# Performance work log

Hardware: AMD Instinct MI355X
Metric: run time of the kernel (lower is better)

Reference implementation:

```python
import jax, jax.numpy as jnp
import numpy as np
import math

B, H, N, D = 4, 8, 2048, 64


def setup_inputs() -> dict:
    key = jax.random.key(0)
    kq, kk, kv = jax.random.split(key, 3)
    q = jax.random.normal(kq, (B, H, N, D), dtype=jnp.float32)
    k = jax.random.normal(kk, (B, H, N, D), dtype=jnp.float32)
    v = jax.random.normal(kv, (B, H, N, D), dtype=jnp.float32)
    return {"q": q, "k": k, "v": v}


def reference(q, k, v):
    # global_attention_Sub: expanded squared L2 distance ||q_i - k_j||^2
    # = qq_i - 2 q_i.k_j + kk_j, then softmax(-dist/sqrt(D)) @ v.
    scale = math.sqrt(q.shape[-1])
    inner = -2.0 * jnp.einsum('bhnd,bhmd->bhnm', q, k)          # [B,H,N,N]
    qq = jnp.sum(q * q, axis=-1, keepdims=True)                  # [B,H,N,1]
    kk = jnp.sum(k * k, axis=-1, keepdims=True)                  # [B,H,N,1]
    diff_sq = qq + inner + jnp.swapaxes(kk, -1, -2)              # [B,H,N,N]
    attn = jax.nn.softmax(-diff_sq / scale, axis=-1)
    x = jnp.einsum('bhnm,bhmd->bhnd', attn, v)                   # [B,H,N,D]
    return jnp.transpose(x, (0, 2, 1, 3))                        # [B,N,H,D]
```

## Files before the change

kernel.cpp:

```cpp
#include <hip/hip_runtime.h>

typedef __bf16 bf16x4 __attribute__((ext_vector_type(4)));
typedef __bf16 bf16x8 __attribute__((ext_vector_type(8)));
typedef float floatx4 __attribute__((ext_vector_type(4)));

constexpr int Bc = 4, Hc = 8, Nc = 2048, Dc = 64;
constexpr int BQ = 128;
constexpr int WQ = 16;
constexpr int TK = 64;
constexpr int NT = Nc / TK;
constexpr int SPS = 72;
constexpr float LOG2E = 1.44269504088896340736f;

constexpr size_t KSW_OFF = 0;
constexpr size_t VSW_OFF = (size_t)32 * NT * 8192;
constexpr size_t KKN_OFF = VSW_OFF * 2;

typedef __attribute__((address_space(1))) const unsigned int gu32;
typedef __attribute__((address_space(3))) unsigned int lu32;
__device__ __forceinline__ void dma16(const void* g, void* l) {
    __builtin_amdgcn_global_load_lds((gu32*)g, (lu32*)l, 16, 0, 0);
}
__device__ __forceinline__ void dma4(const void* g, void* l) {
    __builtin_amdgcn_global_load_lds((gu32*)g, (lu32*)l, 4, 0, 0);
}

__global__ __launch_bounds__(256) void prep_kernel(
    const float* __restrict__ Kg, const float* __restrict__ Vg, char* __restrict__ ws)
{
    __shared__ float sT[64 * 68];
    const int tid = threadIdx.x;
    const int jt = blockIdx.x, bh = blockIdx.y;

    __bf16* Ksw = (__bf16*)(ws + KSW_OFF) + ((size_t)bh * NT + jt) * 4096;
    __bf16* Vsw = (__bf16*)(ws + VSW_OFF) + ((size_t)bh * NT + jt) * 4096;
    float*  kkn = (float*)(ws + KKN_OFF) + (size_t)bh * Nc + jt * 64;
    const size_t tb = ((size_t)bh * Nc + jt * 64) * Dc;

#pragma unroll
    for (int cc = 0; cc < 2; ++cc) {
        const int g   = tid + cc * 256;
        const int key = g >> 3, kcx = g & 7;
        const int kc  = kcx ^ (key & 7);
        const float* src = Kg + tb + key * 64 + kc * 8;
        float4 a = *(const float4*)src;
        float4 b = *(const float4*)(src + 4);
        float ss = a.x*a.x + a.y*a.y + a.z*a.z + a.w*a.w
                 + b.x*b.x + b.y*b.y + b.z*b.z + b.w*b.w;
        ss += __shfl_xor(ss, 1);
        ss += __shfl_xor(ss, 2);
        ss += __shfl_xor(ss, 4);
        if (kcx == 0) kkn[key] = -(ss * 0.125f * LOG2E);
        bf16x8 c8;
        c8[0]=(__bf16)a.x; c8[1]=(__bf16)a.y; c8[2]=(__bf16)a.z; c8[3]=(__bf16)a.w;
        c8[4]=(__bf16)b.x; c8[5]=(__bf16)b.y; c8[6]=(__bf16)b.z; c8[7]=(__bf16)b.w;
        *(bf16x8*)(Ksw + g * 8) = c8;
    }
    {
        const int js = tid >> 2, dc = (tid & 3) * 16;
        const float* vr = Vg + tb + js * 64 + dc;
        float* dst = &sT[js * 68 + dc];
        *(float4*)dst       = *(const float4*)vr;
        *(float4*)(dst + 4) = *(const float4*)(vr + 4);
        *(float4*)(dst + 8) = *(const float4*)(vr + 8);
        *(float4*)(dst + 12)= *(const float4*)(vr + 12);
    }
    __syncthreads();
#pragma unroll
    for (int cc = 0; cc < 2; ++cc) {
        const int g = tid + cc * 256;
        const int d = g >> 3, kcx = g & 7;
        const int kc = kcx ^ (d & 7);
        bf16x8 c8;
#pragma unroll
        for (int e = 0; e < 8; ++e) {
            const int ee = (e + kcx) & 7;
            c8[ee] = (__bf16)sT[(kc * 8 + ee) * 68 + d];
        }
        *(bf16x8*)(Vsw + g * 8) = c8;
    }
}

__global__ __launch_bounds__(512, 4) void attn_kernel(
    const float* __restrict__ Qg, const char* __restrict__ ws, float* __restrict__ Og)
{
    __shared__ __align__(16) __bf16 sK[2][4096];
    __shared__ __align__(16) __bf16 sVall[3 * 4096];
    __shared__ __align__(16) float  skk[2][64];
    __shared__ __align__(16) __bf16 sP[BQ * SPS];
    __shared__ __align__(16) float  sl[BQ];

    const int tid  = threadIdx.x;
    const int wave = tid >> 6;
    const int lane = tid & 63;
    const int qd   = lane >> 4;
    const int c    = lane & 15;

    const int qt = blockIdx.x;
    const int bh = blockIdx.y;

    const char* Kimg = ws + KSW_OFF + (size_t)bh * NT * 8192;
    const char* Vimg = ws + VSW_OFF + (size_t)bh * NT * 8192;
    const float* kkp = (const float*)(ws + KKN_OFF) + (size_t)bh * Nc;

    const float qscale = 0.25f * LOG2E;
    const int i0 = qt * BQ + wave * WQ;

    bf16x8 qf[2];
    {
        const float* qrow = Qg + ((size_t)bh * Nc + i0 + c) * Dc + qd * 8;
#pragma unroll
        for (int ks = 0; ks < 2; ++ks) {
            float4 a = *(const float4*)(qrow + ks * 32);
            float4 b = *(const float4*)(qrow + ks * 32 + 4);
            bf16x8 f;
            f[0] = (__bf16)(a.x * qscale); f[1] = (__bf16)(a.y * qscale);
            f[2] = (__bf16)(a.z * qscale); f[3] = (__bf16)(a.w * qscale);
            f[4] = (__bf16)(b.x * qscale); f[5] = (__bf16)(b.y * qscale);
            f[6] = (__bf16)(b.z * qscale); f[7] = (__bf16)(b.w * qscale);
            qf[ks] = f;
        }
    }

    const int koff0 = c * 64 + ((qd ^ (c & 7)) << 3);
    const int koff1 = c * 64 + (((4 + qd) ^ (c & 7)) << 3);

    floatx4 oacc[4];
#pragma unroll
    for (int dt = 0; dt < 4; ++dt)
#pragma unroll
        for (int e = 0; e < 4; ++e) oacc[dt][e] = 0.f;
    float lp = 0.f;

    __bf16* vprev = &sVall[2 * 4096];
    __bf16* vcur  = &sVall[0];
    __bf16* vnext = &sVall[1 * 4096];

    auto stage = [&](int jt2, int kb, __bf16* vdst) {
        const char* ki = Kimg + (size_t)jt2 * 8192;
        const char* vi = Vimg + (size_t)jt2 * 8192;
        const int off = tid * 16;
        dma16(ki + off, (char*)&sK[kb][0] + off);
        dma16(vi + off, (char*)vdst + off);
        if (wave == 7) dma4(kkp + jt2 * 64 + lane, &skk[kb][0]);
    };

    stage(0, 0, vcur);

    bf16x8 pfp[2];

    for (int jt = 0; jt < NT; ++jt) {
        const int b = jt & 1;
        __syncthreads();
        if (jt + 1 < NT) stage(jt + 1, b ^ 1, vnext);

        floatx4 st[4];
#pragma unroll
        for (int kt = 0; kt < 4; ++kt)
            st[kt] = *(const floatx4*)&skk[b][kt * 16 + qd * 4];
#pragma unroll
        for (int kt = 0; kt < 4; ++kt) {
            const __bf16* kbase = &sK[b][kt * 1024];
            bf16x8 kf0 = *(const bf16x8*)(kbase + koff0);
            bf16x8 kf1 = *(const bf16x8*)(kbase + koff1);
            st[kt] = __builtin_amdgcn_mfma_f32_16x16x32_bf16(kf0, qf[0], st[kt], 0, 0, 0);
            st[kt] = __builtin_amdgcn_mfma_f32_16x16x32_bf16(kf1, qf[1], st[kt], 0, 0, 0);
        }

        if (jt > 0) {
#pragma unroll
            for (int dt = 0; dt < 4; ++dt) {
                const __bf16* vbase = vprev + dt * 1024;
                bf16x8 vf0 = *(const bf16x8*)(vbase + koff0);
                bf16x8 vf1 = *(const bf16x8*)(vbase + koff1);
                oacc[dt] = __builtin_amdgcn_mfma_f32_16x16x32_bf16(pfp[0], vf0, oacc[dt], 0, 0, 0);
                oacc[dt] = __builtin_amdgcn_mfma_f32_16x16x32_bf16(pfp[1], vf1, oacc[dt], 0, 0, 0);
            }
        }

        {
            const int prow = wave * WQ + c;
#pragma unroll
            for (int kt = 0; kt < 4; ++kt) {
                float p0 = __builtin_amdgcn_exp2f(st[kt][0]);
                float p1 = __builtin_amdgcn_exp2f(st[kt][1]);
                float p2 = __builtin_amdgcn_exp2f(st[kt][2]);
                float p3 = __builtin_amdgcn_exp2f(st[kt][3]);
                lp += (p0 + p1) + (p2 + p3);
                bf16x4 pk;
                pk[0] = (__bf16)p0; pk[1] = (__bf16)p1;
                pk[2] = (__bf16)p2; pk[3] = (__bf16)p3;
                *(bf16x4*)&sP[prow * SPS + kt * 16 + qd * 4] = pk;
            }
        }
#pragma unroll
        for (int ks = 0; ks < 2; ++ks)
            pfp[ks] = *(const bf16x8*)&sP[(wave * WQ + c) * SPS + ks * 32 + qd * 8];

        __bf16* t = vprev; vprev = vcur; vcur = vnext; vnext = t;
    }

#pragma unroll
    for (int dt = 0; dt < 4; ++dt) {
        const __bf16* vbase = vprev + dt * 1024;
        bf16x8 vf0 = *(const bf16x8*)(vbase + koff0);
        bf16x8 vf1 = *(const bf16x8*)(vbase + koff1);
        oacc[dt] = __builtin_amdgcn_mfma_f32_16x16x32_bf16(pfp[0], vf0, oacc[dt], 0, 0, 0);
        oacc[dt] = __builtin_amdgcn_mfma_f32_16x16x32_bf16(pfp[1], vf1, oacc[dt], 0, 0, 0);
    }

    {
        float l = lp;
        l += __shfl_xor(l, 16);
        l += __shfl_xor(l, 32);
        if (qd == 0) sl[wave * WQ + c] = l;
    }
    const int b_ = bh >> 3, hh = bh & 7;
    {
        floatx4 lf = *(const floatx4*)&sl[wave * WQ + qd * 4];
#pragma unroll
        for (int r = 0; r < 4; ++r) {
            const float inv = 1.f / lf[r];
            const int i = i0 + qd * 4 + r;
            float* orow = Og + (((size_t)b_ * Nc + i) * Hc + hh) * Dc + c;
#pragma unroll
            for (int dt = 0; dt < 4; ++dt)
                orow[dt * 16] = oacc[dt][r] * inv;
        }
    }
}

extern "C" void kernel_launch(void* const* d_in, const int* in_sizes, int n_in,
                              void* d_out, int out_size, void* d_ws, size_t ws_size,
                              hipStream_t stream) {
    const float* q = (const float*)d_in[0];
    const float* k = (const float*)d_in[1];
    const float* v = (const float*)d_in[2];
    float* out = (float*)d_out;
    char* ws = (char*)d_ws;
    prep_kernel<<<dim3(NT, Bc * Hc), 256, 0, stream>>>(k, v, ws);
    attn_kernel<<<dim3(Nc / BQ, Bc * Hc), 512, 0, stream>>>(q, ws, out);
}
```

Before: 136.9 us.

## Switch attention to 32x32 MFMA with in-register P via permlane32 swap

Moves the attention kernel from 16x16x32 to 32x32x16 bf16 MFMA, with 4 waves of 32 query rows each instead of 8 waves of 16. The probability tile no longer goes through shared memory: it is packed to bf16 and rearranged between lane halves with v_permlane32_swap, then used directly as the A operand of the PV MFMA. The key-norm bias is written by prep in a permuted order matching the 32x32 accumulator layout and read straight from global memory rather than staged through LDS. This removes the sP LDS round trip and the one-tile-delayed PV pipeline, in exchange for more registers per wave and half as many waves per block.

```diff
diff --git a/kernel.cpp b/kernel.cpp
--- a/kernel.cpp
+++ b/kernel.cpp
@@ -1,15 +1,15 @@
 #include <hip/hip_runtime.h>
 
-typedef __bf16 bf16x4 __attribute__((ext_vector_type(4)));
 typedef __bf16 bf16x8 __attribute__((ext_vector_type(8)));
 typedef float floatx4 __attribute__((ext_vector_type(4)));
+typedef float floatx16 __attribute__((ext_vector_type(16)));
+typedef unsigned int uintx4 __attribute__((ext_vector_type(4)));
 
 constexpr int Bc = 4, Hc = 8, Nc = 2048, Dc = 64;
 constexpr int BQ = 128;
-constexpr int WQ = 16;
+constexpr int WQ = 32;
 constexpr int TK = 64;
 constexpr int NT = Nc / TK;
-constexpr int SPS = 72;
 constexpr float LOG2E = 1.44269504088896340736f;
 
 constexpr size_t KSW_OFF = 0;
@@ -21,8 +21,11 @@
 __device__ __forceinline__ void dma16(const void* g, void* l) {
     __builtin_amdgcn_global_load_lds((gu32*)g, (lu32*)l, 16, 0, 0);
 }
-__device__ __forceinline__ void dma4(const void* g, void* l) {
-    __builtin_amdgcn_global_load_lds((gu32*)g, (lu32*)l, 4, 0, 0);
+
+__device__ __forceinline__ unsigned pk2(float lo, float hi) {
+    unsigned short a = __builtin_bit_cast(unsigned short, (__bf16)lo);
+    unsigned short b = __builtin_bit_cast(unsigned short, (__bf16)hi);
+    return (unsigned)a | ((unsigned)b << 16);
 }
 
 __global__ __launch_bounds__(256) void prep_kernel(
@@ -50,7 +53,11 @@
         ss += __shfl_xor(ss, 1);
         ss += __shfl_xor(ss, 2);
         ss += __shfl_xor(ss, 4);
-        if (kcx == 0) kkn[key] = -(ss * 0.125f * LOG2E);
+        if (kcx == 0) {
+            const int k5 = key & 31, kt = key >> 5;
+            const int rlo = k5 & 3, hh = (k5 >> 2) & 1, rhi = k5 >> 3;
+            kkn[kt * 32 + hh * 16 + rhi * 4 + rlo] = -(ss * 0.125f * LOG2E);
+        }
         bf16x8 c8;
         c8[0]=(__bf16)a.x; c8[1]=(__bf16)a.y; c8[2]=(__bf16)a.z; c8[3]=(__bf16)a.w;
         c8[4]=(__bf16)b.x; c8[5]=(__bf16)b.y; c8[6]=(__bf16)b.z; c8[7]=(__bf16)b.w;
@@ -81,20 +88,18 @@
     }
 }
 
-__global__ __launch_bounds__(512, 4) void attn_kernel(
+__global__ __launch_bounds__(256, 4) void attn_kernel(
     const float* __restrict__ Qg, const char* __restrict__ ws, float* __restrict__ Og)
 {
     __shared__ __align__(16) __bf16 sK[2][4096];
-    __shared__ __align__(16) __bf16 sVall[3 * 4096];
-    __shared__ __align__(16) float  skk[2][64];
-    __shared__ __align__(16) __bf16 sP[BQ * SPS];
+    __shared__ __align__(16) __bf16 sV[2][4096];
     __shared__ __align__(16) float  sl[BQ];
 
     const int tid  = threadIdx.x;
     const int wave = tid >> 6;
     const int lane = tid & 63;
-    const int qd   = lane >> 4;
-    const int c    = lane & 15;
+    const int r31  = lane & 31;
+    const int hi   = lane >> 5;
 
     const int qt = blockIdx.x;
     const int bh = blockIdx.y;
@@ -106,13 +111,13 @@
     const float qscale = 0.25f * LOG2E;
     const int i0 = qt * BQ + wave * WQ;
 
-    bf16x8 qf[2];
+    bf16x8 qf[4];
     {
-        const float* qrow = Qg + ((size_t)bh * Nc + i0 + c) * Dc + qd * 8;
-#pragma unroll
-        for (int ks = 0; ks < 2; ++ks) {
-            float4 a = *(const float4*)(qrow + ks * 32);
-            float4 b = *(const float4*)(qrow + ks * 32 + 4);
+        const float* qrow = Qg + ((size_t)bh * Nc + i0 + r31) * Dc + hi * 8;
+#pragma unroll
+        for (int ks = 0; ks < 4; ++ks) {
+            float4 a = *(const float4*)(qrow + ks * 16);
+            float4 b = *(const float4*)(qrow + ks * 16 + 4);
             bf16x8 f;
             f[0] = (__bf16)(a.x * qscale); f[1] = (__bf16)(a.y * qscale);
             f[2] = (__bf16)(a.z * qscale); f[3] = (__bf16)(a.w * qscale);
@@ -122,110 +127,105 @@
         }
     }
 
-    const int koff0 = c * 64 + ((qd ^ (c & 7)) << 3);
-    const int koff1 = c * 64 + (((4 + qd) ^ (c & 7)) << 3);
-
-    floatx4 oacc[4];
-#pragma unroll
-    for (int dt = 0; dt < 4; ++dt)
-#pragma unroll
-        for (int e = 0; e < 4; ++e) oacc[dt][e] = 0.f;
-    float lp = 0.f;
-
-    __bf16* vprev = &sVall[2 * 4096];
-    __bf16* vcur  = &sVall[0];
-    __bf16* vnext = &sVall[1 * 4096];
-
-    auto stage = [&](int jt2, int kb, __bf16* vdst) {
+    int off4[4];
+#pragma unroll
+    for (int ks = 0; ks < 4; ++ks)
+        off4[ks] = r31 * 128 + (((ks * 2 + hi) ^ (r31 & 7)) << 4);
+
+    floatx16 oacc[2];
+#pragma unroll
+    for (int dt = 0; dt < 2; ++dt)
+#pragma unroll
+        for (int e = 0; e < 16; ++e) oacc[dt][e] = 0.f;
+    float lpr = 0.f;
+
+    auto stage = [&](int jt2, int nb) {
         const char* ki = Kimg + (size_t)jt2 * 8192;
         const char* vi = Vimg + (size_t)jt2 * 8192;
         const int off = tid * 16;
-        dma16(ki + off, (char*)&sK[kb][0] + off);
-        dma16(vi + off, (char*)vdst + off);
-        if (wave == 7) dma4(kkp + jt2 * 64 + lane, &skk[kb][0]);
+        dma16(ki + off,        (char*)&sK[nb][0] + off);
+        dma16(ki + off + 4096, (char*)&sK[nb][0] + off + 4096);
+        dma16(vi + off,        (char*)&sV[nb][0] + off);
+        dma16(vi + off + 4096, (char*)&sV[nb][0] + off + 4096);
     };
 
-    stage(0, 0, vcur);
-
-    bf16x8 pfp[2];
+    stage(0, 0);
 
     for (int jt = 0; jt < NT; ++jt) {
         const int b = jt & 1;
         __syncthreads();
-        if (jt + 1 < NT) stage(jt + 1, b ^ 1, vnext);
-
-        floatx4 st[4];
-#pragma unroll
-        for (int kt = 0; kt < 4; ++kt)
-            st[kt] = *(const floatx4*)&skk[b][kt * 16 + qd * 4];
-#pragma unroll
-        for (int kt = 0; kt < 4; ++kt) {
-            const __bf16* kbase = &sK[b][kt * 1024];
-            bf16x8 kf0 = *(const bf16x8*)(kbase + koff0);
-            bf16x8 kf1 = *(const bf16x8*)(kbase + koff1);
-            st[kt] = __builtin_amdgcn_mfma_f32_16x16x32_bf16(kf0, qf[0], st[kt], 0, 0, 0);
-            st[kt] = __builtin_amdgcn_mfma_f32_16x16x32_bf16(kf1, qf[1], st[kt], 0, 0, 0);
-        }
-
-        if (jt > 0) {
-#pragma unroll
-            for (int dt = 0; dt < 4; ++dt) {
-                const __bf16* vbase = vprev + dt * 1024;
-                bf16x8 vf0 = *(const bf16x8*)(vbase + koff0);
-                bf16x8 vf1 = *(const bf16x8*)(vbase + koff1);
-                oacc[dt] = __builtin_amdgcn_mfma_f32_16x16x32_bf16(pfp[0], vf0, oacc[dt], 0, 0, 0);
-                oacc[dt] = __builtin_amdgcn_mfma_f32_16x16x32_bf16(pfp[1], vf1, oacc[dt], 0, 0, 0);
-            }
-        }
-
-        {
-            const int prow = wave * WQ + c;
-#pragma unroll
-            for (int kt = 0; kt < 4; ++kt) {
-                float p0 = __builtin_amdgcn_exp2f(st[kt][0]);
-                float p1 = __builtin_amdgcn_exp2f(st[kt][1]);
-                float p2 = __builtin_amdgcn_exp2f(st[kt][2]);
-                float p3 = __builtin_amdgcn_exp2f(st[kt][3]);
-                lp += (p0 + p1) + (p2 + p3);
-                bf16x4 pk;
-                pk[0] = (__bf16)p0; pk[1] = (__bf16)p1;
-                pk[2] = (__bf16)p2; pk[3] = (__bf16)p3;
-                *(bf16x4*)&sP[prow * SPS + kt * 16 + qd * 4] = pk;
-            }
-        }
-#pragma unroll
-        for (int ks = 0; ks < 2; ++ks)
-            pfp[ks] = *(const bf16x8*)&sP[(wave * WQ + c) * SPS + ks * 32 + qd * 8];
-
-        __bf16* t = vprev; vprev = vcur; vcur = vnext; vnext = t;
-    }
-
-#pragma unroll
-    for (int dt = 0; dt < 4; ++dt) {
-        const __bf16* vbase = vprev + dt * 1024;
-        bf16x8 vf0 = *(const bf16x8*)(vbase + koff0);
-        bf16x8 vf1 = *(const bf16x8*)(vbase + koff1);
-        oacc[dt] = __builtin_amdgcn_mfma_f32_16x16x32_bf16(pfp[0], vf0, oacc[dt], 0, 0, 0);
-        oacc[dt] = __builtin_amdgcn_mfma_f32_16x16x32_bf16(pfp[1], vf1, oacc[dt], 0, 0, 0);
+        if (jt + 1 < NT) stage(jt + 1, b ^ 1);
+
+        floatx16 st[2];
+        const float* kkb = kkp + jt * 64 + hi * 16;
+#pragma unroll
+        for (int kt = 0; kt < 2; ++kt) {
+#pragma unroll
+            for (int gi = 0; gi < 4; ++gi) {
+                floatx4 kv = *(const floatx4*)(kkb + kt * 32 + gi * 4);
+                st[kt][gi * 4 + 0] = kv[0]; st[kt][gi * 4 + 1] = kv[1];
+                st[kt][gi * 4 + 2] = kv[2]; st[kt][gi * 4 + 3] = kv[3];
+            }
+        }
+
+        const char* kb = (const char*)&sK[b][0];
+#pragma unroll
+        for (int kt = 0; kt < 2; ++kt)
+#pragma unroll
+            for (int ks = 0; ks < 4; ++ks) {
+                bf16x8 kf = *(const bf16x8*)(kb + kt * 4096 + off4[ks]);
+                st[kt] = __builtin_amdgcn_mfma_f32_32x32x16_bf16(kf, qf[ks], st[kt], 0, 0, 0);
+            }
+
+        const char* vb = (const char*)&sV[b][0];
+#pragma unroll
+        for (int kt = 0; kt < 2; ++kt) {
+            float p[16];
+#pragma unroll
+            for (int r = 0; r < 16; ++r) {
+                p[r] = __builtin_amdgcn_exp2f(st[kt][r]);
+                lpr += p[r];
+            }
+            unsigned w[4][2];
+#pragma unroll
+            for (int g = 0; g < 4; ++g) {
+                w[g][0] = pk2(p[4 * g + 0], p[4 * g + 1]);
+                w[g][1] = pk2(p[4 * g + 2], p[4 * g + 3]);
+            }
+#pragma unroll
+            for (int sub = 0; sub < 2; ++sub) {
+                unsigned a0 = w[2 * sub][0],     a1 = w[2 * sub][1];
+                unsigned b0 = w[2 * sub + 1][0], b1 = w[2 * sub + 1][1];
+                asm("v_permlane32_swap_b32 %0, %1" : "+v"(a0), "+v"(b0));
+                asm("v_permlane32_swap_b32 %0, %1" : "+v"(a1), "+v"(b1));
+                uintx4 u; u[0] = a0; u[1] = a1; u[2] = b0; u[3] = b1;
+                bf16x8 pa = __builtin_bit_cast(bf16x8, u);
+                const int ks = kt * 2 + sub;
+#pragma unroll
+                for (int dt = 0; dt < 2; ++dt) {
+                    bf16x8 vf = *(const bf16x8*)(vb + dt * 4096 + off4[ks]);
+                    oacc[dt] = __builtin_amdgcn_mfma_f32_32x32x16_bf16(pa, vf, oacc[dt], 0, 0, 0);
+                }
+            }
+        }
     }
 
     {
-        float l = lp;
-        l += __shfl_xor(l, 16);
-        l += __shfl_xor(l, 32);
-        if (qd == 0) sl[wave * WQ + c] = l;
+        float l = lpr + __shfl_xor(lpr, 32);
+        if (!hi) sl[wave * 32 + r31] = l;
     }
     const int b_ = bh >> 3, hh = bh & 7;
-    {
-        floatx4 lf = *(const floatx4*)&sl[wave * WQ + qd * 4];
-#pragma unroll
-        for (int r = 0; r < 4; ++r) {
-            const float inv = 1.f / lf[r];
-            const int i = i0 + qd * 4 + r;
-            float* orow = Og + (((size_t)b_ * Nc + i) * Hc + hh) * Dc + c;
-#pragma unroll
-            for (int dt = 0; dt < 4; ++dt)
-                orow[dt * 16] = oacc[dt][r] * inv;
+#pragma unroll
+    for (int g = 0; g < 4; ++g) {
+        floatx4 lf = *(const floatx4*)&sl[wave * 32 + 8 * g + 4 * hi];
+#pragma unroll
+        for (int rlo = 0; rlo < 4; ++rlo) {
+            const float inv = 1.f / lf[rlo];
+            const int i = i0 + 8 * g + 4 * hi + rlo;
+            float* orow = Og + (((size_t)b_ * Nc + i) * Hc + hh) * Dc + r31;
+            const int r = 4 * g + rlo;
+            orow[0]  = oacc[0][r] * inv;
+            orow[32] = oacc[1][r] * inv;
         }
     }
 }
@@ -239,5 +239,5 @@
     float* out = (float*)d_out;
     char* ws = (char*)d_ws;
     prep_kernel<<<dim3(NT, Bc * Hc), 256, 0, stream>>>(k, v, ws);
-    attn_kernel<<<dim3(Nc / BQ, Bc * Hc), 512, 0, stream>>>(q, ws, out);
-}
+    attn_kernel<<<dim3(Nc / BQ, Bc * Hc), 256, 0, stream>>>(q, ws, out);
+}
```

Measured after the change: 155.9 us. 1.14x slower.
